# Performance work log

Measured on AMD Instinct MI355X. Metric: run time of the kernel, lower is better.

The kernel has to match this reference:

```python
import jax, jax.numpy as jnp
import numpy as np

NUM_HEADS = 16
HEAD_DIM = 80
HIDDEN = 1280
SEQ = 3072
NUM_SEGS = 6  # 6 packed images of 512 patches each


def rotate_half(x):
    x1, x2 = jnp.split(x, 2, axis=-1)
    return jnp.concatenate([-x2, x1], axis=-1)


def setup_inputs() -> dict:
    key = jax.random.key(0)
    ks = jax.random.split(key, 6)
    hidden_states = jax.random.normal(ks[0], (SEQ, HIDDEN), dtype=jnp.float32)
    # RoPE tables as in Qwen-VL vision: freqs over half the head_dim, duplicated
    half = HEAD_DIM // 2
    inv_freq = 1.0 / (10000.0 ** (jnp.arange(half, dtype=jnp.float32) / half))
    pos = jnp.arange(SEQ, dtype=jnp.float32)[:, None]
    freqs = pos * inv_freq[None, :]                      # (SEQ, half)
    emb = jnp.concatenate([freqs, freqs], axis=-1)       # (SEQ, HEAD_DIM)
    cos = jnp.cos(emb)
    sin = jnp.sin(emb)
    # Packed segment boundaries: [0, 512, 1024, ..., 3072]
    cu_seqlens = jnp.arange(0, SEQ + 1, SEQ // NUM_SEGS, dtype=jnp.int32)
    scale = 0.02
    w_qkv = jax.random.normal(ks[1], (3 * HIDDEN, HIDDEN), dtype=jnp.float32) * scale
    b_qkv = jax.random.normal(ks[2], (3 * HIDDEN,), dtype=jnp.float32) * scale
    w_proj = jax.random.normal(ks[3], (HIDDEN, HIDDEN), dtype=jnp.float32) * scale
    b_proj = jax.random.normal(ks[4], (HIDDEN,), dtype=jnp.float32) * scale
    return {
        "hidden_states": hidden_states, "cos": cos, "sin": sin,
        "w_qkv": w_qkv, "b_qkv": b_qkv, "w_proj": w_proj, "b_proj": b_proj,
        "cu_seqlens": cu_seqlens,
    }


def reference(hidden_states, cos, sin, w_qkv, b_qkv, w_proj, b_proj, cu_seqlens):
    S, H = hidden_states.shape
    nh, hd = NUM_HEADS, H // NUM_HEADS

    # Fused QKV projection: (S, 3H) -> q, k, v each (S, nh, hd)
    qkv = hidden_states @ w_qkv.T + b_qkv
    qkv = qkv.reshape(S, 3, nh, hd)
    q, k, v = qkv[:, 0], qkv[:, 1], qkv[:, 2]

    # Inline RoPE on q/k (cos/sin broadcast over heads)
    c = cos[:, None, :]
    s = sin[:, None, :]
    q = q * c + rotate_half(q) * s
    k = k * c + rotate_half(k) * s

    # Original casts fp32 -> fp16 for the flash attention kernel
    q16 = q.astype(jnp.float16)
    k16 = k.astype(jnp.float16)
    v16 = v.astype(jnp.float16)

    # Varlen masking: tokens attend only within their own packed segment
    tok = jnp.arange(S)
    seg = jnp.searchsorted(cu_seqlens, tok, side="right")  # (S,)
    same_seg = seg[:, None] == seg[None, :]                 # (S, S)

    scale = hd ** (-0.5)
    # Scores accumulated in fp32 (as flash attention does internally)
    scores = jnp.einsum("qhd,khd->hqk", q16, k16,
                        preferred_element_type=jnp.float32) * scale
    scores = jnp.where(same_seg[None], scores, jnp.finfo(jnp.float32).min)
    weights = jax.nn.softmax(scores, axis=-1).astype(jnp.float16)  # (nh, S, S)

    attn = jnp.einsum("hqk,khd->qhd", weights, v16)  # (S, nh, hd) fp16
    attn = attn.astype(jnp.float32).reshape(S, H)
    return attn @ w_proj.T + b_proj
```

## Files before the change

### kernel.cpp

```cpp
#include <hip/hip_runtime.h>

typedef _Float16 f16;
typedef _Float16 half8 __attribute__((ext_vector_type(8)));
typedef _Float16 half4 __attribute__((ext_vector_type(4)));
typedef float f32x4 __attribute__((ext_vector_type(4)));

__device__ __forceinline__ void gld_lds16(const void* g, void* l) {
  __builtin_amdgcn_global_load_lds((const __attribute__((address_space(1))) void*)g,
                                   (__attribute__((address_space(3))) void*)l, 16, 0, 0);
}

template <int CTRL>
__device__ __forceinline__ float dppf(float x) {
  return __builtin_bit_cast(float,
      __builtin_amdgcn_mov_dpp(__builtin_bit_cast(int, x), CTRL, 0xf, 0xf, true));
}
__device__ __forceinline__ float dpp_max16(float v) {
  v = fmaxf(v, dppf<0xB1>(v));
  v = fmaxf(v, dppf<0x4E>(v));
  v = fmaxf(v, dppf<0x128>(v));
  v = fmaxf(v, dppf<0x140>(v));
  return v;
}
__device__ __forceinline__ float dpp_sum16(float v) {
  v += dppf<0xB1>(v);
  v += dppf<0x4E>(v);
  v += dppf<0x128>(v);
  v += dppf<0x140>(v);
  return v;
}

__global__ void cvt_all(const float* __restrict__ hid, const float* __restrict__ wq,
                        const float* __restrict__ wp, f16* __restrict__ hid16,
                        f16* __restrict__ wq16, f16* __restrict__ wp16) {
  int b = blockIdx.x;
  const float* in;
  f16* out;
  int i;
  if (b < 3840) { in = hid; out = hid16; i = b * 256 + threadIdx.x; }
  else if (b < 8640) { in = wq; out = wq16; i = (b - 3840) * 256 + threadIdx.x; }
  else { in = wp; out = wp16; i = (b - 8640) * 256 + threadIdx.x; }
  float4 v = ((const float4*)in)[i];
  half4 o;
  o.x = (f16)v.x; o.y = (f16)v.y; o.z = (f16)v.z; o.w = (f16)v.w;
  ((half4*)out)[i] = o;
}

__global__ __launch_bounds__(256, 2) void gemm240(const f16* __restrict__ A,
                                                  const f16* __restrict__ B,
                                                  const float* __restrict__ bias,
                                                  f16* __restrict__ C) {
  __shared__ f16 S[40960];
  char* Sb = (char*)S;
  const int tid = threadIdx.x, lane = tid & 63, wid = tid >> 6;
  const int lm = lane & 15, q4 = lane >> 4;
  const int wm = wid >> 1, wn = wid & 1;
  const int swz = ((int)blockIdx.x & 7) * 60 + ((int)blockIdx.x >> 3);
  const int bm = (swz % 24) * 128, bn = (swz / 24) * 192;

  const int ch = ((lane & 7) ^ (lane >> 3)) << 3;
  uint32_t aoff[4], boff[6];
#pragma unroll
  for (int j = 0; j < 4; j++)
    aoff[j] = (uint32_t)((bm + (j * 4 + wid) * 8 + (lane >> 3)) * 1280 + ch);
#pragma unroll
  for (int i = 0; i < 6; i++)
    boff[i] = (uint32_t)((bn + wid * 48 + i * 8 + (lane >> 3)) * 1280 + ch);

  const int xr = (lm & 7) << 4;
  int aro[4][2], bro[6][2];
#pragma unroll
  for (int f = 0; f < 4; f++)
#pragma unroll
    for (int ks = 0; ks < 2; ks++)
      aro[f][ks] = (wm * 64 + f * 16 + lm) * 128 + ((ks * 64 + q4 * 16) ^ xr);
#pragma unroll
  for (int n = 0; n < 6; n++)
#pragma unroll
    for (int ks = 0; ks < 2; ks++)
      bro[n][ks] = (wn * 96 + n * 16 + lm) * 128 + ((ks * 64 + q4 * 16) ^ xr);

  f32x4 acc[4][6] = {};

  {
#pragma unroll
    for (int j = 0; j < 4; j++)
      gld_lds16(A + aoff[j], Sb + (j * 4 + wid) * 1024);
#pragma unroll
    for (int i = 0; i < 6; i++)
      gld_lds16(B + boff[i], Sb + 32768 + (wid * 6 + i) * 1024);
    gld_lds16(A + aoff[0] + 64, Sb + 16384 + wid * 1024);
    gld_lds16(A + aoff[2] + 64, Sb + 16384 + (8 + wid) * 1024);
#pragma unroll
    for (int i = 0; i < 6; i++)
      gld_lds16(B + boff[i] + 64, Sb + 32768 + 24576 + (wid * 6 + i) * 1024);
    asm volatile("s_waitcnt vmcnt(8)" ::: "memory");
    __builtin_amdgcn_s_barrier();
  }

  constexpr int NT = 20;
  for (int t = 0; t < NT; ++t) {
    const int p = t & 1;
    char* Ab = Sb + p * 16384;
    char* Bb = Sb + 32768 + p * 24576;
    char* An = Sb + (p ^ 1) * 16384;
    const int k1 = (t + 1) * 64, k2 = (t + 2) * 64;

    half8 a0[2][2], bf[6][2];
#pragma unroll
    for (int f = 0; f < 2; f++)
#pragma unroll
      for (int ks = 0; ks < 2; ks++)
        a0[f][ks] = *(const half8*)(Ab + aro[f][ks]);
#pragma unroll
    for (int n = 0; n < 6; n++)
#pragma unroll
      for (int ks = 0; ks < 2; ks++)
        bf[n][ks] = *(const half8*)(Bb + bro[n][ks]);
    if (t + 1 < NT) {
      gld_lds16(A + aoff[1] + k1, An + (4 + wid) * 1024);
      gld_lds16(A + aoff[3] + k1, An + (12 + wid) * 1024);
    }
    __builtin_amdgcn_s_setprio(1);
#pragma unroll
    for (int ks = 0; ks < 2; ks++)
#pragma unroll
      for (int f = 0; f < 2; f++)
#pragma unroll
        for (int n = 0; n < 6; n++)
          acc[f][n] =
              __builtin_amdgcn_mfma_f32_16x16x32_f16(a0[f][ks], bf[n][ks], acc[f][n], 0, 0, 0);
    __builtin_amdgcn_s_setprio(0);
    __builtin_amdgcn_sched_barrier(0);
    asm volatile("s_waitcnt lgkmcnt(0)" ::: "memory");
    __builtin_amdgcn_s_barrier();

#pragma unroll
    for (int f = 0; f < 2; f++)
#pragma unroll
      for (int ks = 0; ks < 2; ks++)
        a0[f][ks] = *(const half8*)(Ab + aro[2 + f][ks]);
    if (t + 2 < NT) {
      gld_lds16(A + aoff[0] + k2, Ab + wid * 1024);
      gld_lds16(A + aoff[2] + k2, Ab + (8 + wid) * 1024);
#pragma unroll
      for (int i = 0; i < 6; i++)
        gld_lds16(B + boff[i] + k2, Bb + (wid * 6 + i) * 1024);
    }
    __builtin_amdgcn_s_setprio(1);
#pragma unroll
    for (int ks = 0; ks < 2; ks++)
#pragma unroll
      for (int f = 0; f < 2; f++)
#pragma unroll
        for (int n = 0; n < 6; n++)
          acc[2 + f][n] = __builtin_amdgcn_mfma_f32_16x16x32_f16(a0[f][ks], bf[n][ks],
                                                                 acc[2 + f][n], 0, 0, 0);
    __builtin_amdgcn_s_setprio(0);
    __builtin_amdgcn_sched_barrier(0);
    if (t + 2 < NT) {
      asm volatile("s_waitcnt vmcnt(8)" ::: "memory");
    } else {
      asm volatile("s_waitcnt vmcnt(0)" ::: "memory");
    }
    asm volatile("s_waitcnt lgkmcnt(0)" ::: "memory");
    __builtin_amdgcn_s_barrier();
  }

#pragma unroll
  for (int f = 0; f < 4; f++)
#pragma unroll
    for (int n = 0; n < 6; n++) {
      const int gc = bn + wn * 96 + n * 16 + lm;
      const float bb = bias[gc];
      const int gr0 = bm + wm * 64 + f * 16 + q4 * 4;
#pragma unroll
      for (int r = 0; r < 4; r++)
        C[(size_t)(gr0 + r) * 3840 + gc] = (f16)(acc[f][n][r] + bb);
    }
}

template <bool OUT_F16>
__global__ __launch_bounds__(256, 2) void gemm_bt64(const f16* __restrict__ A,
                                                    const f16* __restrict__ B,
                                                    const float* __restrict__ bias,
                                                    void* __restrict__ Cout,
                                                    int K, int lda, int ldb, int ldc) {
  __shared__ f16 As[64 * 32];
  __shared__ f16 Bs[128 * 32];
  const int tid = threadIdx.x, lane = tid & 63, wave = tid >> 6;
  const int bm = blockIdx.x * 64, bn = blockIdx.y * 128;
  const int wm = (wave & 1) * 32, wn = (wave >> 1) * 64;
  const int lm = lane & 15, kq = (lane >> 4) * 8;
  const int arow = tid >> 2, acol = (tid & 3) * 8;

  const f16* Ab = A + (size_t)(bm + arow) * lda + acol;
  const f16* Bb = B + (size_t)(bn + arow) * ldb + acol;
  f16* AsW = As + wave * 512;
  f16* BsW = Bs + wave * 512;

  f32x4 acc[2][4] = {};
  for (int k0 = 0; k0 < K; k0 += 32) {
    gld_lds16(Ab + k0, AsW);
    gld_lds16(Bb + k0, BsW);
    gld_lds16(Bb + (size_t)64 * ldb + k0, BsW + 2048);
    __syncthreads();
    half8 af[2], bf[4];
#pragma unroll
    for (int mt = 0; mt < 2; mt++) af[mt] = *(const half8*)&As[(wm + 16 * mt + lm) * 32 + kq];
#pragma unroll
    for (int nt = 0; nt < 4; nt++) bf[nt] = *(const half8*)&Bs[(wn + 16 * nt + lm) * 32 + kq];
#pragma unroll
    for (int mt = 0; mt < 2; mt++)
#pragma unroll
      for (int nt = 0; nt < 4; nt++)
        acc[mt][nt] = __builtin_amdgcn_mfma_f32_16x16x32_f16(af[mt], bf[nt], acc[mt][nt], 0, 0, 0);
    __syncthreads();
  }
  const int q4 = lane >> 4;
#pragma unroll
  for (int mt = 0; mt < 2; mt++)
#pragma unroll
    for (int nt = 0; nt < 4; nt++)
#pragma unroll
      for (int r = 0; r < 4; r++) {
        int gr = bm + wm + 16 * mt + 4 * q4 + r;
        int gc = bn + wn + 16 * nt + lm;
        float v = acc[mt][nt][r] + bias[gc];
        if (OUT_F16)
          ((f16*)Cout)[(size_t)gr * ldc + gc] = (f16)v;
        else
          ((float*)Cout)[(size_t)gr * ldc + gc] = v;
      }
}

__global__ void rope_transpose(f16* __restrict__ qkv, const float* __restrict__ cosb,
                               const float* __restrict__ sinb, f16* __restrict__ vt) {
  __shared__ f16 tile[64][72];
  const int b = blockIdx.x;
  if (b < 1920) {
    int idx = b * 256 + threadIdx.x;
    int c = idx % 5;
    int t = idx / 5;
    int h = t % 16; t /= 16;
    int qk = t & 1;
    int s = t >> 1;
    size_t base = (size_t)s * 3840 + qk * 1280 + h * 80 + c * 8;
    half8 x = *(half8*)&qkv[base];
    half8 y = *(half8*)&qkv[base + 40];
    const float* cp = cosb + s * 80 + c * 8;
    const float* sp = sinb + s * 80 + c * 8;
    half8 ox, oy;
#pragma unroll
    for (int i = 0; i < 8; i++) {
      float cs = cp[i], sn = sp[i];
      float xf = (float)x[i], yf = (float)y[i];
      ox[i] = (f16)(xf * cs - yf * sn);
      oy[i] = (f16)(yf * cs + xf * sn);
    }
    *(half8*)&qkv[base] = ox;
    *(half8*)&qkv[base + 40] = oy;
  } else {
    const int bb = b - 1920;
    const int bs = (bb % 48) * 64;
    const int bd = (bb / 48) * 64;
    const int r = threadIdx.x >> 2, c = (threadIdx.x & 3) * 16;
    *(uint4*)&tile[r][c] = *(const uint4*)&qkv[(size_t)(bs + r) * 3840 + 2560 + bd + c];
    *(uint4*)&tile[r][c + 8] = *(const uint4*)&qkv[(size_t)(bs + r) * 3840 + 2560 + bd + c + 8];
    __syncthreads();
    f16 tmp[16];
#pragma unroll
    for (int i = 0; i < 16; i++) tmp[i] = tile[c + i][r];
    *(uint4*)&vt[(size_t)(bd + r) * 3072 + bs + c] = *(uint4*)&tmp[0];
    *(uint4*)&vt[(size_t)(bd + r) * 3072 + bs + c + 8] = *(uint4*)&tmp[8];
  }
}

__global__ __launch_bounds__(256, 3) void flash_attn6(const f16* __restrict__ qkv,
                                                      const f16* __restrict__ vt,
                                                      f16* __restrict__ attn) {
  __shared__ f16 S[25088];
  const int tid = threadIdx.x, lane = tid & 63, wave = tid >> 6;
  const int lm = lane & 15, q4 = lane >> 4;
  const int h = blockIdx.x, g = blockIdx.z;
  const int qbase = g * 512 + blockIdx.y * 64 + wave * 16;
  f16* P = S + 20480 + wave * 1152;
  const half8 hz = {};

  const f16* qrow = qkv + (size_t)(qbase + lm) * 3840 + h * 80;
  half8 qf[3];
  qf[0] = *(const half8*)(qrow + q4 * 8);
  qf[1] = *(const half8*)(qrow + 32 + q4 * 8);
  qf[2] = (q4 < 2) ? *(const half8*)(qrow + 64 + q4 * 8) : hz;

  const bool isK = wave < 2;
  const f16* gsrc = isK ? qkv : vt;
  const uint32_t gstep = isK ? (uint32_t)(64 * 3840) : 64u;
  const int cbase = (wave & 1) * 5;
  const uint32_t ldsoff = (isK ? 0u : 5120u) + (uint32_t)cbase * 512u;
  uint32_t goff[5];
#pragma unroll
  for (int i = 0; i < 5; i++) {
    int t = (cbase + i) * 1024 + lane * 16;
    if (isK) {
      int row = t / 160, colb = t % 160;
      goff[i] = (uint32_t)((g * 512 + row) * 3840 + 1280 + h * 80 + (colb >> 1));
    } else {
      int vd = t >> 7, vsb = t & 127;
      int vsrc = vsb ^ ((vd & 7) << 4);
      goff[i] = (uint32_t)((h * 80 + vd) * 3072 + g * 512 + (vsrc >> 1));
    }
  }

  f32x4 oacc[5] = {};
  float mprev[4] = {-1e30f, -1e30f, -1e30f, -1e30f};
  float lsum[4] = {0.f, 0.f, 0.f, 0.f};
  const float sc = 0.11180339887498949f * 1.4426950408889634f;

#pragma unroll
  for (int i = 0; i < 5; i++) gld_lds16(gsrc + goff[i], S + ldsoff + i * 512);
  __syncthreads();

  for (int jj = 0; jj < 8; jj++) {
    const int p = jj & 1;
    f16* Kb = S + p * 10240;
    f16* Vb = Kb + 5120;
    if (jj < 7) {
#pragma unroll
      for (int i = 0; i < 5; i++)
        gld_lds16(gsrc + goff[i] + (uint32_t)(jj + 1) * gstep,
                  S + (p ^ 1) * 10240 + ldsoff + i * 512);
    }

    f32x4 sacc[4] = {};
#pragma unroll
    for (int ks = 0; ks < 3; ks++) {
      half8 bk[4];
#pragma unroll
      for (int nt = 0; nt < 4; nt++)
        bk[nt] = (ks < 2 || q4 < 2)
                     ? *(const half8*)&Kb[(16 * nt + lm) * 80 + 32 * ks + q4 * 8]
                     : hz;
#pragma unroll
      for (int nt = 0; nt < 4; nt++)
        sacc[nt] = __builtin_amdgcn_mfma_f32_16x16x32_f16(qf[ks], bk[nt], sacc[nt], 0, 0, 0);
    }

    float mnew[4], alpha[4], rs[4];
#pragma unroll
    for (int r = 0; r < 4; r++) {
      float v = fmaxf(fmaxf(sacc[0][r], sacc[1][r]), fmaxf(sacc[2][r], sacc[3][r]));
      v = dpp_max16(v);
      mnew[r] = fmaxf(mprev[r], v * sc);
      alpha[r] = __builtin_exp2f(mprev[r] - mnew[r]);
      mprev[r] = mnew[r];
      rs[r] = 0.f;
    }
#pragma unroll
    for (int nt = 0; nt < 4; nt++)
#pragma unroll
      for (int r = 0; r < 4; r++) {
        float pp = __builtin_exp2f(sacc[nt][r] * sc - mnew[r]);
        sacc[nt][r] = pp;
        rs[r] += pp;
      }
#pragma unroll
    for (int r = 0; r < 4; r++) {
      float v = dpp_sum16(rs[r]);
      lsum[r] = alpha[r] * lsum[r] + v;
#pragma unroll
      for (int nt2 = 0; nt2 < 5; nt2++) oacc[nt2][r] *= alpha[r];
    }

#pragma unroll
    for (int nt = 0; nt < 4; nt++)
#pragma unroll
      for (int r = 0; r < 4; r++)
        P[(4 * q4 + r) * 72 + 16 * nt + lm] = (f16)sacc[nt][r];

#pragma unroll
    for (int ks = 0; ks < 2; ks++) {
      half8 ap = *(const half8*)&P[lm * 72 + ks * 32 + q4 * 8];
      half8 bv[5];
#pragma unroll
      for (int nt2 = 0; nt2 < 5; nt2++) {
        int row = 16 * nt2 + lm;
        bv[nt2] = *(const half8*)&Vb[row * 64 + ((ks * 32 + q4 * 8) ^ ((row & 7) << 3))];
      }
#pragma unroll
      for (int nt2 = 0; nt2 < 5; nt2++)
        oacc[nt2] = __builtin_amdgcn_mfma_f32_16x16x32_f16(ap, bv[nt2], oacc[nt2], 0, 0, 0);
    }

    __syncthreads();
  }

#pragma unroll
  for (int r = 0; r < 4; r++) {
    float inv = 1.0f / lsum[r];
    int s = qbase + 4 * q4 + r;
#pragma unroll
    for (int nt2 = 0; nt2 < 5; nt2++)
      attn[(size_t)s * 1280 + h * 80 + 16 * nt2 + lm] = (f16)(oacc[nt2][r] * inv);
  }
}

extern "C" void kernel_launch(void* const* d_in, const int* in_sizes, int n_in,
                              void* d_out, int out_size, void* d_ws, size_t ws_size,
                              hipStream_t stream) {
  const float* hidden = (const float*)d_in[0];
  const float* cosb   = (const float*)d_in[1];
  const float* sinb   = (const float*)d_in[2];
  const float* w_qkv  = (const float*)d_in[3];
  const float* b_qkv  = (const float*)d_in[4];
  const float* w_proj = (const float*)d_in[5];
  const float* b_proj = (const float*)d_in[6];

  char* ws = (char*)d_ws;
  f16* hidden16 = (f16*)(ws + 0);
  f16* wqkv16   = (f16*)(ws + 7864320);
  f16* wproj16  = (f16*)(ws + 17694720);
  f16* qkv16    = (f16*)(ws + 20971520);
  f16* attn16   = (f16*)(ws + 44564480);
  f16* vt16     = hidden16;

  cvt_all<<<10240, 256, 0, stream>>>(hidden, w_qkv, w_proj, hidden16, wqkv16, wproj16);

  gemm240<<<480, 256, 0, stream>>>(hidden16, wqkv16, b_qkv, qkv16);

  rope_transpose<<<2880, 256, 0, stream>>>(qkv16, cosb, sinb, vt16);

  flash_attn6<<<dim3(16, 8, 6), 256, 0, stream>>>(qkv16, vt16, attn16);

  gemm_bt64<false><<<dim3(48, 10), 256, 0, stream>>>(attn16, wproj16, b_proj, d_out,
                                                     1280, 1280, 1280, 1280);
}
```

Before: 186.0 us.

## Fuse fp32-to-fp16 conversion of QKV GEMM operands into the GEMM loader

The QKV GEMM now reads fp32 hidden states and weights directly, converts them to fp16 in registers and writes them into swizzled LDS, replacing the separate conversion pass over hidden and w_qkv. Only w_proj is still converted by a standalone kernel. This removes a launch and the fp16 round trip through global memory, but it trades asynchronous global-to-LDS loads for register-staged loads. Each GEMM block also re-reads and re-converts fp32 tiles, which doubles the bytes per tile and adds register pressure and VALU work inside the pipelined loop.

```diff
diff --git a/kernel.cpp b/kernel.cpp
--- a/kernel.cpp
+++ b/kernel.cpp
@@ -30,24 +30,23 @@
   return v;
 }
 
-__global__ void cvt_all(const float* __restrict__ hid, const float* __restrict__ wq,
-                        const float* __restrict__ wp, f16* __restrict__ hid16,
-                        f16* __restrict__ wq16, f16* __restrict__ wp16) {
-  int b = blockIdx.x;
-  const float* in;
-  f16* out;
-  int i;
-  if (b < 3840) { in = hid; out = hid16; i = b * 256 + threadIdx.x; }
-  else if (b < 8640) { in = wq; out = wq16; i = (b - 3840) * 256 + threadIdx.x; }
-  else { in = wp; out = wp16; i = (b - 8640) * 256 + threadIdx.x; }
-  float4 v = ((const float4*)in)[i];
+__device__ __forceinline__ void cvtw(void* dst, float4 x, float4 y) {
+  half8 o;
+  o[0] = (f16)x.x; o[1] = (f16)x.y; o[2] = (f16)x.z; o[3] = (f16)x.w;
+  o[4] = (f16)y.x; o[5] = (f16)y.y; o[6] = (f16)y.z; o[7] = (f16)y.w;
+  *(half8*)dst = o;
+}
+
+__global__ void cvt_proj(const float* __restrict__ wp, f16* __restrict__ wp16) {
+  int i = blockIdx.x * 256 + threadIdx.x;
+  float4 v = ((const float4*)wp)[i];
   half4 o;
   o.x = (f16)v.x; o.y = (f16)v.y; o.z = (f16)v.z; o.w = (f16)v.w;
-  ((half4*)out)[i] = o;
-}
-
-__global__ __launch_bounds__(256, 2) void gemm240(const f16* __restrict__ A,
-                                                  const f16* __restrict__ B,
+  ((half4*)wp16)[i] = o;
+}
+
+__global__ __launch_bounds__(256, 2) void gemm240(const float* __restrict__ A32,
+                                                  const float* __restrict__ B32,
                                                   const float* __restrict__ bias,
                                                   f16* __restrict__ C) {
   __shared__ f16 S[40960];
@@ -58,14 +57,15 @@
   const int swz = ((int)blockIdx.x & 7) * 60 + ((int)blockIdx.x >> 3);
   const int bm = (swz % 24) * 128, bn = (swz / 24) * 192;
 
-  const int ch = ((lane & 7) ^ (lane >> 3)) << 3;
+  const int l8 = lane >> 3;
+  const int lw = l8 * 128 + (((lane & 7) * 16) ^ (l8 << 4));
   uint32_t aoff[4], boff[6];
 #pragma unroll
   for (int j = 0; j < 4; j++)
-    aoff[j] = (uint32_t)((bm + (j * 4 + wid) * 8 + (lane >> 3)) * 1280 + ch);
+    aoff[j] = (uint32_t)((bm + (j * 4 + wid) * 8 + l8) * 1280 + (lane & 7) * 8);
 #pragma unroll
   for (int i = 0; i < 6; i++)
-    boff[i] = (uint32_t)((bn + wid * 48 + i * 8 + (lane >> 3)) * 1280 + ch);
+    boff[i] = (uint32_t)((bn + (wid * 6 + i) * 8 + l8) * 1280 + (lane & 7) * 8);
 
   const int xr = (lm & 7) << 4;
   int aro[4][2], bro[6][2];
@@ -84,18 +84,27 @@
 
   {
 #pragma unroll
-    for (int j = 0; j < 4; j++)
-      gld_lds16(A + aoff[j], Sb + (j * 4 + wid) * 1024);
-#pragma unroll
-    for (int i = 0; i < 6; i++)
-      gld_lds16(B + boff[i], Sb + 32768 + (wid * 6 + i) * 1024);
-    gld_lds16(A + aoff[0] + 64, Sb + 16384 + wid * 1024);
-    gld_lds16(A + aoff[2] + 64, Sb + 16384 + (8 + wid) * 1024);
-#pragma unroll
-    for (int i = 0; i < 6; i++)
-      gld_lds16(B + boff[i] + 64, Sb + 32768 + 24576 + (wid * 6 + i) * 1024);
-    asm volatile("s_waitcnt vmcnt(8)" ::: "memory");
-    __builtin_amdgcn_s_barrier();
+    for (int j = 0; j < 4; j++) {
+      const float4* s = (const float4*)(A32 + aoff[j]);
+      cvtw(Sb + (j * 4 + wid) * 1024 + lw, s[0], s[1]);
+    }
+#pragma unroll
+    for (int i = 0; i < 6; i++) {
+      const float4* s = (const float4*)(B32 + boff[i]);
+      cvtw(Sb + 32768 + (wid * 6 + i) * 1024 + lw, s[0], s[1]);
+    }
+    {
+      const float4* s0 = (const float4*)(A32 + aoff[0] + 64);
+      cvtw(Sb + 16384 + wid * 1024 + lw, s0[0], s0[1]);
+      const float4* s2 = (const float4*)(A32 + aoff[2] + 64);
+      cvtw(Sb + 16384 + (8 + wid) * 1024 + lw, s2[0], s2[1]);
+    }
+#pragma unroll
+    for (int i = 0; i < 6; i++) {
+      const float4* s = (const float4*)(B32 + boff[i] + 64);
+      cvtw(Sb + 32768 + 24576 + (wid * 6 + i) * 1024 + lw, s[0], s[1]);
+    }
+    __syncthreads();
   }
 
   constexpr int NT = 20;
@@ -104,8 +113,15 @@
     char* Ab = Sb + p * 16384;
     char* Bb = Sb + 32768 + p * 24576;
     char* An = Sb + (p ^ 1) * 16384;
-    const int k1 = (t + 1) * 64, k2 = (t + 2) * 64;
-
+    const uint32_t k1 = (uint32_t)(t + 1) * 64, k2 = (uint32_t)(t + 2) * 64;
+
+    float4 sx[2], sy[2];
+    if (t + 1 < NT) {
+      const float4* s1 = (const float4*)(A32 + aoff[1] + k1);
+      sx[0] = s1[0]; sy[0] = s1[1];
+      const float4* s3 = (const float4*)(A32 + aoff[3] + k1);
+      sx[1] = s3[0]; sy[1] = s3[1];
+    }
     half8 a0[2][2], bf[6][2];
 #pragma unroll
     for (int f = 0; f < 2; f++)
@@ -117,10 +133,6 @@
 #pragma unroll
       for (int ks = 0; ks < 2; ks++)
         bf[n][ks] = *(const half8*)(Bb + bro[n][ks]);
-    if (t + 1 < NT) {
-      gld_lds16(A + aoff[1] + k1, An + (4 + wid) * 1024);
-      gld_lds16(A + aoff[3] + k1, An + (12 + wid) * 1024);
-    }
     __builtin_amdgcn_s_setprio(1);
 #pragma unroll
     for (int ks = 0; ks < 2; ks++)
@@ -131,22 +143,31 @@
           acc[f][n] =
               __builtin_amdgcn_mfma_f32_16x16x32_f16(a0[f][ks], bf[n][ks], acc[f][n], 0, 0, 0);
     __builtin_amdgcn_s_setprio(0);
+    if (t + 1 < NT) {
+      cvtw(An + (4 + wid) * 1024 + lw, sx[0], sy[0]);
+      cvtw(An + (12 + wid) * 1024 + lw, sx[1], sy[1]);
+    }
     __builtin_amdgcn_sched_barrier(0);
     asm volatile("s_waitcnt lgkmcnt(0)" ::: "memory");
     __builtin_amdgcn_s_barrier();
 
+    float4 ax[2], ay[2], bx[6], by[6];
+    if (t + 2 < NT) {
+      const float4* s0 = (const float4*)(A32 + aoff[0] + k2);
+      ax[0] = s0[0]; ay[0] = s0[1];
+      const float4* s2 = (const float4*)(A32 + aoff[2] + k2);
+      ax[1] = s2[0]; ay[1] = s2[1];
+#pragma unroll
+      for (int i = 0; i < 6; i++) {
+        const float4* s = (const float4*)(B32 + boff[i] + k2);
+        bx[i] = s[0]; by[i] = s[1];
+      }
+    }
 #pragma unroll
     for (int f = 0; f < 2; f++)
 #pragma unroll
       for (int ks = 0; ks < 2; ks++)
         a0[f][ks] = *(const half8*)(Ab + aro[2 + f][ks]);
-    if (t + 2 < NT) {
-      gld_lds16(A + aoff[0] + k2, Ab + wid * 1024);
-      gld_lds16(A + aoff[2] + k2, Ab + (8 + wid) * 1024);
-#pragma unroll
-      for (int i = 0; i < 6; i++)
-        gld_lds16(B + boff[i] + k2, Bb + (wid * 6 + i) * 1024);
-    }
     __builtin_amdgcn_s_setprio(1);
 #pragma unroll
     for (int ks = 0; ks < 2; ks++)
@@ -157,12 +178,14 @@
           acc[2 + f][n] = __builtin_amdgcn_mfma_f32_16x16x32_f16(a0[f][ks], bf[n][ks],
                                                                  acc[2 + f][n], 0, 0, 0);
     __builtin_amdgcn_s_setprio(0);
+    if (t + 2 < NT) {
+      cvtw(Ab + wid * 1024 + lw, ax[0], ay[0]);
+      cvtw(Ab + (8 + wid) * 1024 + lw, ax[1], ay[1]);
+#pragma unroll
+      for (int i = 0; i < 6; i++)
+        cvtw(Bb + (wid * 6 + i) * 1024 + lw, bx[i], by[i]);
+    }
     __builtin_amdgcn_sched_barrier(0);
-    if (t + 2 < NT) {
-      asm volatile("s_waitcnt vmcnt(8)" ::: "memory");
-    } else {
-      asm volatile("s_waitcnt vmcnt(0)" ::: "memory");
-    }
     asm volatile("s_waitcnt lgkmcnt(0)" ::: "memory");
     __builtin_amdgcn_s_barrier();
   }
@@ -417,16 +440,14 @@
   const float* b_proj = (const float*)d_in[6];
 
   char* ws = (char*)d_ws;
-  f16* hidden16 = (f16*)(ws + 0);
-  f16* wqkv16   = (f16*)(ws + 7864320);
   f16* wproj16  = (f16*)(ws + 17694720);
   f16* qkv16    = (f16*)(ws + 20971520);
   f16* attn16   = (f16*)(ws + 44564480);
-  f16* vt16     = hidden16;
-
-  cvt_all<<<10240, 256, 0, stream>>>(hidden, w_qkv, w_proj, hidden16, wqkv16, wproj16);
-
-  gemm240<<<480, 256, 0, stream>>>(hidden16, wqkv16, b_qkv, qkv16);
+  f16* vt16     = (f16*)(ws + 0);
+
+  cvt_proj<<<1600, 256, 0, stream>>>(w_proj, wproj16);
+
+  gemm240<<<480, 256, 0, stream>>>(hidden, w_qkv, b_qkv, qkv16);
 
   rope_transpose<<<2880, 256, 0, stream>>>(qkv16, cosb, sinb, vt16);
 
```

New measurement: 208.3 us. 12.0% more time.

## Load K fragments directly from global memory in flash attention, stage only V in LDS

Applied to the files above, without the earlier changes.

The attention kernel no longer stages K tiles through shared memory. Each wave reads its K MFMA operands straight from global memory, and only two waves stream V tiles into a smaller LDS double buffer. This cuts LDS footprint and LDS traffic for K, which could allow higher occupancy. In exchange, every wave issues redundant uncoalesced-ish global loads for K that are not prefetched ahead of use, so latency may be exposed. The change to the GEMM B offset is arithmetically identical.

```diff
diff --git a/kernel.cpp b/kernel.cpp
--- a/kernel.cpp
+++ b/kernel.cpp
@@ -65,7 +65,7 @@
     aoff[j] = (uint32_t)((bm + (j * 4 + wid) * 8 + (lane >> 3)) * 1280 + ch);
 #pragma unroll
   for (int i = 0; i < 6; i++)
-    boff[i] = (uint32_t)((bn + wid * 48 + i * 8 + (lane >> 3)) * 1280 + ch);
+    boff[i] = (uint32_t)((bn + (wid * 6 + i) * 8 + (lane >> 3)) * 1280 + ch);
 
   const int xr = (lm & 7) << 4;
   int aro[4][2], bro[6][2];
@@ -276,15 +276,15 @@
   }
 }
 
-__global__ __launch_bounds__(256, 3) void flash_attn6(const f16* __restrict__ qkv,
+__global__ __launch_bounds__(256, 3) void flash_attn7(const f16* __restrict__ qkv,
                                                       const f16* __restrict__ vt,
                                                       f16* __restrict__ attn) {
-  __shared__ f16 S[25088];
+  __shared__ f16 S[14848];
   const int tid = threadIdx.x, lane = tid & 63, wave = tid >> 6;
   const int lm = lane & 15, q4 = lane >> 4;
   const int h = blockIdx.x, g = blockIdx.z;
   const int qbase = g * 512 + blockIdx.y * 64 + wave * 16;
-  f16* P = S + 20480 + wave * 1152;
+  f16* P = S + 10240 + wave * 1152;
   const half8 hz = {};
 
   const f16* qrow = qkv + (size_t)(qbase + lm) * 3840 + h * 80;
@@ -293,23 +293,16 @@
   qf[1] = *(const half8*)(qrow + 32 + q4 * 8);
   qf[2] = (q4 < 2) ? *(const half8*)(qrow + 64 + q4 * 8) : hz;
 
-  const bool isK = wave < 2;
-  const f16* gsrc = isK ? qkv : vt;
-  const uint32_t gstep = isK ? (uint32_t)(64 * 3840) : 64u;
-  const int cbase = (wave & 1) * 5;
-  const uint32_t ldsoff = (isK ? 0u : 5120u) + (uint32_t)cbase * 512u;
-  uint32_t goff[5];
+  const f16* kb = qkv + (size_t)(g * 512 + lm) * 3840 + 1280 + h * 80 + q4 * 8;
+
+  const int cbase = wave * 5;
+  uint32_t vgo[5];
 #pragma unroll
   for (int i = 0; i < 5; i++) {
     int t = (cbase + i) * 1024 + lane * 16;
-    if (isK) {
-      int row = t / 160, colb = t % 160;
-      goff[i] = (uint32_t)((g * 512 + row) * 3840 + 1280 + h * 80 + (colb >> 1));
-    } else {
-      int vd = t >> 7, vsb = t & 127;
-      int vsrc = vsb ^ ((vd & 7) << 4);
-      goff[i] = (uint32_t)((h * 80 + vd) * 3072 + g * 512 + (vsrc >> 1));
-    }
+    int vd = t >> 7, vsb = t & 127;
+    int vsrc = vsb ^ ((vd & 7) << 4);
+    vgo[i] = (uint32_t)((h * 80 + vd) * 3072 + g * 512 + (vsrc >> 1));
   }
 
   f32x4 oacc[5] = {};
@@ -317,34 +310,38 @@
   float lsum[4] = {0.f, 0.f, 0.f, 0.f};
   const float sc = 0.11180339887498949f * 1.4426950408889634f;
 
-#pragma unroll
-  for (int i = 0; i < 5; i++) gld_lds16(gsrc + goff[i], S + ldsoff + i * 512);
+  if (wave < 2) {
+#pragma unroll
+    for (int i = 0; i < 5; i++) gld_lds16(vt + vgo[i], S + cbase * 512 + i * 512);
+  }
   __syncthreads();
 
   for (int jj = 0; jj < 8; jj++) {
     const int p = jj & 1;
-    f16* Kb = S + p * 10240;
-    f16* Vb = Kb + 5120;
-    if (jj < 7) {
+    f16* Vb = S + p * 5120;
+    if (jj < 7 && wave < 2) {
 #pragma unroll
       for (int i = 0; i < 5; i++)
-        gld_lds16(gsrc + goff[i] + (uint32_t)(jj + 1) * gstep,
-                  S + (p ^ 1) * 10240 + ldsoff + i * 512);
-    }
+        gld_lds16(vt + vgo[i] + (uint32_t)(jj + 1) * 64,
+                  S + (p ^ 1) * 5120 + cbase * 512 + i * 512);
+    }
+
+    const f16* kj = kb + (size_t)jj * (64 * 3840);
+    half8 bk[3][4];
+#pragma unroll
+    for (int ks = 0; ks < 3; ks++)
+#pragma unroll
+      for (int nt = 0; nt < 4; nt++)
+        bk[ks][nt] = (ks < 2 || q4 < 2)
+                         ? *(const half8*)(kj + (size_t)(16 * nt) * 3840 + 32 * ks)
+                         : hz;
 
     f32x4 sacc[4] = {};
 #pragma unroll
-    for (int ks = 0; ks < 3; ks++) {
-      half8 bk[4];
+    for (int ks = 0; ks < 3; ks++)
 #pragma unroll
       for (int nt = 0; nt < 4; nt++)
-        bk[nt] = (ks < 2 || q4 < 2)
-                     ? *(const half8*)&Kb[(16 * nt + lm) * 80 + 32 * ks + q4 * 8]
-                     : hz;
-#pragma unroll
-      for (int nt = 0; nt < 4; nt++)
-        sacc[nt] = __builtin_amdgcn_mfma_f32_16x16x32_f16(qf[ks], bk[nt], sacc[nt], 0, 0, 0);
-    }
+        sacc[nt] = __builtin_amdgcn_mfma_f32_16x16x32_f16(qf[ks], bk[ks][nt], sacc[nt], 0, 0, 0);
 
     float mnew[4], alpha[4], rs[4];
 #pragma unroll
@@ -430,7 +427,7 @@
 
   rope_transpose<<<2880, 256, 0, stream>>>(qkv16, cosb, sinb, vt16);
 
-  flash_attn6<<<dim3(16, 8, 6), 256, 0, stream>>>(qkv16, vt16, attn16);
+  flash_attn7<<<dim3(16, 8, 6), 256, 0, stream>>>(qkv16, vt16, attn16);
 
   gemm_bt64<false><<<dim3(48, 10), 256, 0, stream>>>(attn16, wproj16, b_proj, d_out,
                                                      1280, 1280, 1280, 1280);
```

Result: slower. 201.8 us (+8.5%).

## Split attention KV range across wave pairs with LDS merge of partial softmax

Applied to the files above, without the earlier changes.

The flash attention kernel now handles 32 queries per block instead of 64. Each pair of waves splits the 512-key segment into two halves, uses 32-key tiles, and merges the partial max, sum and output through shared memory at the end. This doubles the grid to 1536 blocks to improve occupancy and latency hiding. It adds a final LDS reduction and sync, and uses less MFMA work per tile. The gemm B-offset edit is an equivalent rewrite of the same index.

```diff
diff --git a/kernel.cpp b/kernel.cpp
--- a/kernel.cpp
+++ b/kernel.cpp
@@ -65,7 +65,7 @@
     aoff[j] = (uint32_t)((bm + (j * 4 + wid) * 8 + (lane >> 3)) * 1280 + ch);
 #pragma unroll
   for (int i = 0; i < 6; i++)
-    boff[i] = (uint32_t)((bn + wid * 48 + i * 8 + (lane >> 3)) * 1280 + ch);
+    boff[i] = (uint32_t)((bn + (wid * 6 + i) * 8 + (lane >> 3)) * 1280 + ch);
 
   const int xr = (lm & 7) << 4;
   int aro[4][2], bro[6][2];
@@ -276,39 +276,42 @@
   }
 }
 
-__global__ __launch_bounds__(256, 3) void flash_attn6(const f16* __restrict__ qkv,
+__global__ __launch_bounds__(256, 3) void flash_attn8(const f16* __restrict__ qkv,
                                                       const f16* __restrict__ vt,
                                                       f16* __restrict__ attn) {
-  __shared__ f16 S[25088];
+  __shared__ f16 S[23040];
   const int tid = threadIdx.x, lane = tid & 63, wave = tid >> 6;
   const int lm = lane & 15, q4 = lane >> 4;
-  const int h = blockIdx.x, g = blockIdx.z;
-  const int qbase = g * 512 + blockIdx.y * 64 + wave * 16;
-  f16* P = S + 20480 + wave * 1152;
+  const int qg = wave >> 1, hf = wave & 1;
+  const int hh = blockIdx.x, g = blockIdx.z;
+  const int qbase = g * 512 + blockIdx.y * 32 + qg * 16;
+  const int kvbase = g * 512 + hf * 256;
+  f16* P = S + 20480 + wave * 640;
   const half8 hz = {};
 
-  const f16* qrow = qkv + (size_t)(qbase + lm) * 3840 + h * 80;
+  const f16* qrow = qkv + (size_t)(qbase + lm) * 3840 + hh * 80;
   half8 qf[3];
   qf[0] = *(const half8*)(qrow + q4 * 8);
   qf[1] = *(const half8*)(qrow + 32 + q4 * 8);
   qf[2] = (q4 < 2) ? *(const half8*)(qrow + 64 + q4 * 8) : hz;
 
-  const bool isK = wave < 2;
+  const bool isK = (wave & 1) == 0;
+  const int hfs = wave >> 1;
+  const int kvs = g * 512 + hfs * 256;
   const f16* gsrc = isK ? qkv : vt;
-  const uint32_t gstep = isK ? (uint32_t)(64 * 3840) : 64u;
-  const int cbase = (wave & 1) * 5;
-  const uint32_t ldsoff = (isK ? 0u : 5120u) + (uint32_t)cbase * 512u;
+  const uint32_t gstep = isK ? (uint32_t)(32 * 3840) : 32u;
+  const uint32_t ldsoff = (uint32_t)(hfs * 5120 + (isK ? 0 : 2560));
   uint32_t goff[5];
 #pragma unroll
   for (int i = 0; i < 5; i++) {
-    int t = (cbase + i) * 1024 + lane * 16;
+    int t = i * 1024 + lane * 16;
     if (isK) {
       int row = t / 160, colb = t % 160;
-      goff[i] = (uint32_t)((g * 512 + row) * 3840 + 1280 + h * 80 + (colb >> 1));
+      goff[i] = (uint32_t)((kvs + row) * 3840 + 1280 + hh * 80 + (colb >> 1));
     } else {
-      int vd = t >> 7, vsb = t & 127;
-      int vsrc = vsb ^ ((vd & 7) << 4);
-      goff[i] = (uint32_t)((h * 80 + vd) * 3072 + g * 512 + (vsrc >> 1));
+      int vd = t >> 6, vsb = t & 63;
+      int vsrc = vsb ^ ((vd & 3) << 4);
+      goff[i] = (uint32_t)((hh * 80 + vd) * 3072 + kvs + (vsrc >> 1));
     }
   }
 
@@ -323,8 +326,8 @@
 
   for (int jj = 0; jj < 8; jj++) {
     const int p = jj & 1;
-    f16* Kb = S + p * 10240;
-    f16* Vb = Kb + 5120;
+    f16* Kb = S + p * 10240 + hf * 5120;
+    f16* Vb = Kb + 2560;
     if (jj < 7) {
 #pragma unroll
       for (int i = 0; i < 5; i++)
@@ -332,24 +335,24 @@
                   S + (p ^ 1) * 10240 + ldsoff + i * 512);
     }
 
-    f32x4 sacc[4] = {};
+    f32x4 sacc[2] = {};
 #pragma unroll
     for (int ks = 0; ks < 3; ks++) {
-      half8 bk[4];
-#pragma unroll
-      for (int nt = 0; nt < 4; nt++)
+      half8 bk[2];
+#pragma unroll
+      for (int nt = 0; nt < 2; nt++)
         bk[nt] = (ks < 2 || q4 < 2)
                      ? *(const half8*)&Kb[(16 * nt + lm) * 80 + 32 * ks + q4 * 8]
                      : hz;
 #pragma unroll
-      for (int nt = 0; nt < 4; nt++)
+      for (int nt = 0; nt < 2; nt++)
         sacc[nt] = __builtin_amdgcn_mfma_f32_16x16x32_f16(qf[ks], bk[nt], sacc[nt], 0, 0, 0);
     }
 
     float mnew[4], alpha[4], rs[4];
 #pragma unroll
     for (int r = 0; r < 4; r++) {
-      float v = fmaxf(fmaxf(sacc[0][r], sacc[1][r]), fmaxf(sacc[2][r], sacc[3][r]));
+      float v = fmaxf(sacc[0][r], sacc[1][r]);
       v = dpp_max16(v);
       mnew[r] = fmaxf(mprev[r], v * sc);
       alpha[r] = __builtin_exp2f(mprev[r] - mnew[r]);
@@ -357,7 +360,7 @@
       rs[r] = 0.f;
     }
 #pragma unroll
-    for (int nt = 0; nt < 4; nt++)
+    for (int nt = 0; nt < 2; nt++)
 #pragma unroll
       for (int r = 0; r < 4; r++) {
         float pp = __builtin_exp2f(sacc[nt][r] * sc - mnew[r]);
@@ -373,19 +376,18 @@
     }
 
 #pragma unroll
-    for (int nt = 0; nt < 4; nt++)
+    for (int nt = 0; nt < 2; nt++)
 #pragma unroll
       for (int r = 0; r < 4; r++)
-        P[(4 * q4 + r) * 72 + 16 * nt + lm] = (f16)sacc[nt][r];
-
-#pragma unroll
-    for (int ks = 0; ks < 2; ks++) {
-      half8 ap = *(const half8*)&P[lm * 72 + ks * 32 + q4 * 8];
+        P[(4 * q4 + r) * 40 + 16 * nt + lm] = (f16)sacc[nt][r];
+
+    {
+      half8 ap = *(const half8*)&P[lm * 40 + q4 * 8];
       half8 bv[5];
 #pragma unroll
       for (int nt2 = 0; nt2 < 5; nt2++) {
         int row = 16 * nt2 + lm;
-        bv[nt2] = *(const half8*)&Vb[row * 64 + ((ks * 32 + q4 * 8) ^ ((row & 7) << 3))];
+        bv[nt2] = *(const half8*)&Vb[row * 32 + ((q4 * 8) ^ ((row & 3) << 3))];
       }
 #pragma unroll
       for (int nt2 = 0; nt2 < 5; nt2++)
@@ -395,13 +397,37 @@
     __syncthreads();
   }
 
-#pragma unroll
-  for (int r = 0; r < 4; r++) {
-    float inv = 1.0f / lsum[r];
-    int s = qbase + 4 * q4 + r;
+  float* scr = (float*)S;
+  if (hf == 1) {
 #pragma unroll
     for (int nt2 = 0; nt2 < 5; nt2++)
-      attn[(size_t)s * 1280 + h * 80 + 16 * nt2 + lm] = (f16)(oacc[nt2][r] * inv);
+      *(f32x4*)&scr[qg * 1792 + nt2 * 256 + lane * 4] = oacc[nt2];
+    f32x4 mv, lv;
+#pragma unroll
+    for (int r = 0; r < 4; r++) { mv[r] = mprev[r]; lv[r] = lsum[r]; }
+    *(f32x4*)&scr[qg * 1792 + 1280 + lane * 4] = mv;
+    *(f32x4*)&scr[qg * 1792 + 1536 + lane * 4] = lv;
+  }
+  __syncthreads();
+  if (hf == 0) {
+    f32x4 m2 = *(const f32x4*)&scr[qg * 1792 + 1280 + lane * 4];
+    f32x4 l2 = *(const f32x4*)&scr[qg * 1792 + 1536 + lane * 4];
+    f32x4 o2[5];
+#pragma unroll
+    for (int nt2 = 0; nt2 < 5; nt2++)
+      o2[nt2] = *(const f32x4*)&scr[qg * 1792 + nt2 * 256 + lane * 4];
+#pragma unroll
+    for (int r = 0; r < 4; r++) {
+      float M = fmaxf(mprev[r], m2[r]);
+      float a1 = __builtin_exp2f(mprev[r] - M);
+      float a2 = __builtin_exp2f(m2[r] - M);
+      float inv = 1.0f / (a1 * lsum[r] + a2 * l2[r]);
+      int s = qbase + 4 * q4 + r;
+#pragma unroll
+      for (int nt2 = 0; nt2 < 5; nt2++)
+        attn[(size_t)s * 1280 + hh * 80 + 16 * nt2 + lm] =
+            (f16)((a1 * oacc[nt2][r] + a2 * o2[nt2][r]) * inv);
+    }
   }
 }
 
@@ -430,7 +456,7 @@
 
   rope_transpose<<<2880, 256, 0, stream>>>(qkv16, cosb, sinb, vt16);
 
-  flash_attn6<<<dim3(16, 8, 6), 256, 0, stream>>>(qkv16, vt16, attn16);
+  flash_attn8<<<dim3(16, 16, 6), 256, 0, stream>>>(qkv16, vt16, attn16);
 
   gemm_bt64<false><<<dim3(48, 10), 256, 0, stream>>>(attn16, wproj16, b_proj, d_out,
                                                      1280, 1280, 1280, 1280);
```

Result: slower. 194.2 us (+4.4%).
